# Performance work log

Measured on AMD Instinct MI355X. Metric: run time of the kernel, lower is better.

Reference implementation:

```python
import jax, jax.numpy as jnp
import numpy as np

N_ATOMS = 100000
N_PAIRS = 3200000
N_PROP = 16
N_BASIS = 10
W = 16  # MLP width for pp/pi/ii nodes


def setup_inputs() -> dict:
    key = jax.random.key(0)
    ks = jax.random.split(key, 16)
    s = 0.1
    inp = {
        "ind_2": jax.random.randint(ks[0], (N_PAIRS, 2), 0, N_ATOMS),
        "p1": jax.random.normal(ks[1], (N_ATOMS, N_PROP), dtype=jnp.float32),
        "basis": jax.random.normal(ks[2], (N_PAIRS, N_BASIS), dtype=jnp.float32),
        # pp_pre: [16,16], bias=True
        "Wpre0": jax.random.normal(ks[3], (N_PROP, W), dtype=jnp.float32) * s,
        "bpre0": jnp.zeros((W,), dtype=jnp.float32),
        "Wpre1": jax.random.normal(ks[4], (W, W), dtype=jnp.float32) * s,
        "bpre1": jnp.zeros((W,), dtype=jnp.float32),
        # pi: input 2*W -> W -> W*n_basis, bias=True
        "Wpi0": jax.random.normal(ks[5], (2 * W, W), dtype=jnp.float32) * s,
        "bpi0": jnp.zeros((W,), dtype=jnp.float32),
        "Wpi1": jax.random.normal(ks[6], (W, W * N_BASIS), dtype=jnp.float32) * s,
        "bpi1": jnp.zeros((W * N_BASIS,), dtype=jnp.float32),
        # ii: [16,16], bias=False
        "Wii0": jax.random.normal(ks[7], (W, W), dtype=jnp.float32) * s,
        "Wii1": jax.random.normal(ks[8], (W, W), dtype=jnp.float32) * s,
        # pp_post: [16,16], bias=False
        "Wpost0": jax.random.normal(ks[9], (W, W), dtype=jnp.float32) * s,
        "Wpost1": jax.random.normal(ks[10], (W, W), dtype=jnp.float32) * s,
    }
    return inp


def reference(ind_2, p1, basis, Wpre0, bpre0, Wpre1, bpre1,
              Wpi0, bpi0, Wpi1, bpi1, Wii0, Wii1, Wpost0, Wpost1):
    act = jnp.tanh
    n_atoms = p1.shape[0]
    # pp_pre: per-atom FF (activation on every dense, bias=True)
    p1_in = act(p1 @ Wpre0 + bpre0)
    p1_in = act(p1_in @ Wpre1 + bpre1)
    # PI: gather pair endpoints, concat, MLP, contract with radial basis
    h = jnp.concatenate([p1_in[ind_2[:, 0]], p1_in[ind_2[:, 1]]], axis=-1)  # (P, 2W)
    h = act(h @ Wpi0 + bpi0)                                                # (P, W)
    h = act(h @ Wpi1 + bpi1)                                                # (P, W*n_basis)
    h = h.reshape(h.shape[0], -1, basis.shape[-1])                          # (P, W, n_basis)
    i_pair = jnp.einsum('pcb,pb->pc', h, basis)                             # (P, W)
    # II: pair-mixing FF (bias=False)
    i_pair = act(i_pair @ Wii0)
    i_pair = act(i_pair @ Wii1)
    # IP: scatter-sum pair features back to atoms at ind_2[:,0]
    p_sum = jax.ops.segment_sum(i_pair, ind_2[:, 0], num_segments=n_atoms)  # (A, W)
    # pp_post (bias=False)
    p1_new = act(p_sum @ Wpost0)
    p1_new = act(p1_new @ Wpost1)
    return (p1_new, i_pair)
```

## Files before the change

### kernel.cpp

```cpp
#include <hip/hip_runtime.h>

#define N_ATOMS 100000
#define N_PAIRS 3200000
#define N_PROP 16
#define N_BASIS 10
#define W 16
#define NSUP (N_PAIRS / 32)
#define SCAN_BLK 1024
#define NB ((N_ATOMS + SCAN_BLK - 1) / SCAN_BLK)
#define SC 2.88539008177792681f

typedef short  s16x8  __attribute__((ext_vector_type(8)));
typedef float  f32x4  __attribute__((ext_vector_type(4)));
typedef float  f32x16 __attribute__((ext_vector_type(16)));

__device__ __forceinline__ float tanh_pre(float y) {
    float e = __builtin_amdgcn_exp2f(y);
    return 1.0f - 2.0f * __builtin_amdgcn_rcpf(e + 1.0f);
}
__device__ __forceinline__ float fast_tanh(float x) {
    float e = __builtin_amdgcn_exp2f(x * SC);
    return 1.0f - 2.0f * __builtin_amdgcn_rcpf(e + 1.0f);
}
__device__ __forceinline__ unsigned short bf16r(float f) {
    union { float f; unsigned u; } v; v.f = f;
    unsigned r = v.u + 0x7FFFu + ((v.u >> 16) & 1u);
    return (unsigned short)(r >> 16);
}
__device__ __forceinline__ unsigned cvt_pk_bf16(float a, float b) {
    unsigned r;
    asm("v_cvt_pk_bf16_f32 %0, %1, %2" : "=v"(r) : "v"(a), "v"(b));
    return r;
}
__device__ __forceinline__ float bitf(unsigned u) {
    union { unsigned u; float f; } v; v.u = u; return v.f;
}

__global__ __launch_bounds__(256) void k_pp_pre(
    const float* __restrict__ p1,
    const float* __restrict__ W0, const float* __restrict__ b0,
    const float* __restrict__ W1, const float* __restrict__ b1,
    const float* __restrict__ Wpi0, const float* __restrict__ bpi0,
    float* __restrict__ ytop, float* __restrict__ ybot)
{
    int a = blockIdx.x * 256 + threadIdx.x;
    if (a >= N_ATOMS) return;
    const float4* src = reinterpret_cast<const float4*>(p1 + (size_t)a * N_PROP);
    float4 v0 = src[0], v1 = src[1], v2 = src[2], v3 = src[3];
    float x[N_PROP] = {v0.x,v0.y,v0.z,v0.w, v1.x,v1.y,v1.z,v1.w,
                       v2.x,v2.y,v2.z,v2.w, v3.x,v3.y,v3.z,v3.w};
    float h[W];
#pragma unroll
    for (int c = 0; c < W; ++c) h[c] = b0[c];
#pragma unroll
    for (int k = 0; k < N_PROP; ++k)
#pragma unroll
        for (int c = 0; c < W; ++c) h[c] += x[k] * W0[k*W + c];
#pragma unroll
    for (int c = 0; c < W; ++c) h[c] = fast_tanh(h[c]);
    float y[W];
#pragma unroll
    for (int c = 0; c < W; ++c) y[c] = b1[c];
#pragma unroll
    for (int k = 0; k < W; ++k)
#pragma unroll
        for (int c = 0; c < W; ++c) y[c] += h[k] * W1[k*W + c];
    float t[W];
#pragma unroll
    for (int c = 0; c < W; ++c) t[c] = fast_tanh(y[c]);

    float yt[W], yb[W];
#pragma unroll
    for (int c = 0; c < W; ++c) { yt[c] = bpi0[c]; yb[c] = 0.0f; }
#pragma unroll
    for (int k = 0; k < W; ++k)
#pragma unroll
        for (int c = 0; c < W; ++c) {
            yt[c] += t[k] * Wpi0[k*W + c];
            yb[c] += t[k] * Wpi0[(W + k)*W + c];
        }
    float4* dt = reinterpret_cast<float4*>(ytop + (size_t)a * W);
    float4* db = reinterpret_cast<float4*>(ybot + (size_t)a * W);
#pragma unroll
    for (int q = 0; q < 4; ++q) {
        dt[q] = make_float4(SC*yt[4*q], SC*yt[4*q+1], SC*yt[4*q+2], SC*yt[4*q+3]);
        db[q] = make_float4(SC*yb[4*q], SC*yb[4*q+1], SC*yb[4*q+2], SC*yb[4*q+3]);
    }
}

__global__ __launch_bounds__(256) void k_pair_mfma(
    const int*   __restrict__ ind2,
    const float* __restrict__ basis,
    const float* __restrict__ ytop,
    const float* __restrict__ ybot,
    const float* __restrict__ Wpi1, const float* __restrict__ bpi1,
    const float* __restrict__ Wii0, const float* __restrict__ Wii1,
    float* __restrict__ i_pair_out)
{
    __shared__ s16x8 aw_lds[5][2][32];
    __shared__ s16x8 ab_lds[5][2][32];

    const int lane = threadIdx.x & 63;
    const int wv   = threadIdx.x >> 6;
    const int col  = lane & 31;
    const int h    = lane >> 5;

    for (int e = threadIdx.x; e < 320; e += 256) {
        int T = e >> 6, hh = (e >> 5) & 1, row = e & 31;
        int colW = (4*(row >> 3) + (row & 3)) * N_BASIS + 2*T + ((row >> 2) & 1);
        s16x8 wfrag, bfrag;
#pragma unroll
        for (int j = 0; j < 8; ++j) {
            int k = 8*hh + j;
            wfrag[j] = (short)bf16r(SC * Wpi1[k*(W*N_BASIS) + colW]);
            bfrag[j] = (short)((k == 0) ? bf16r(SC * bpi1[colW]) : 0);
        }
        aw_lds[T][hh][row] = wfrag;
        ab_lds[T][hh][row] = bfrag;
    }

    s16x8 a3, a4;
#pragma unroll
    for (int j = 0; j < 8; ++j) {
        int k = 8*h + j;
        a3[j] = (short)(col < W ? bf16r(SC * Wii0[k*W + col]) : 0);
        a4[j] = (short)(col < W ? bf16r(SC * Wii1[k*W + col]) : 0);
    }
    s16x8 Bones = {0,0,0,0,0,0,0,0};
    if (h == 0) Bones[0] = (short)0x3F80;

    __syncthreads();

    const int stride = gridDim.x * 4;
    int sup = blockIdx.x * 4 + wv;
    if (sup >= NSUP) return;
    const int2* ind2v = reinterpret_cast<const int2*>(ind2);

    int2 ij = ind2v[(size_t)sup * 32 + col];
    f32x4 yt0 = *reinterpret_cast<const f32x4*>(ytop + (size_t)ij.x * W + 8*h);
    f32x4 yt1 = *reinterpret_cast<const f32x4*>(ytop + (size_t)ij.x * W + 8*h + 4);
    f32x4 yb0 = *reinterpret_cast<const f32x4*>(ybot + (size_t)ij.y * W + 8*h);
    f32x4 yb1 = *reinterpret_cast<const f32x4*>(ybot + (size_t)ij.y * W + 8*h + 4);

    for (; sup < NSUP; sup += stride) {
        const int p0 = sup * 32;
        const int p  = p0 + col;
        const int nsup = (sup + stride < NSUP) ? (sup + stride) : sup;

        int2 nij = ind2v[(size_t)nsup * 32 + col];

        float h0[8];
#pragma unroll
        for (int j = 0; j < 4; ++j) h0[j]     = tanh_pre(yt0[j] + yb0[j]);
#pragma unroll
        for (int j = 0; j < 4; ++j) h0[4 + j] = tanh_pre(yt1[j] + yb1[j]);
        unsigned w0h = cvt_pk_bf16(h0[0], h0[1]);
        unsigned w1h = cvt_pk_bf16(h0[2], h0[3]);
        unsigned w2h = cvt_pk_bf16(h0[4], h0[5]);
        unsigned w3h = cvt_pk_bf16(h0[6], h0[7]);
        unsigned w0l = cvt_pk_bf16(h0[0] - bitf(w0h << 16), h0[1] - bitf(w0h & 0xFFFF0000u));
        unsigned w1l = cvt_pk_bf16(h0[2] - bitf(w1h << 16), h0[3] - bitf(w1h & 0xFFFF0000u));
        unsigned w2l = cvt_pk_bf16(h0[4] - bitf(w2h << 16), h0[5] - bitf(w2h & 0xFFFF0000u));
        unsigned w3l = cvt_pk_bf16(h0[6] - bitf(w3h << 16), h0[7] - bitf(w3h & 0xFFFF0000u));
        union { unsigned u[4]; s16x8 v; } BH, BL;
        BH.u[0] = w0h; BH.u[1] = w1h; BH.u[2] = w2h; BH.u[3] = w3h;
        BL.u[0] = w0l; BL.u[1] = w1l; BL.u[2] = w2l; BL.u[3] = w3l;
        s16x8 B2h = BH.v, B2l = BL.v;

        const float2* bb = reinterpret_cast<const float2*>(basis + (size_t)p * N_BASIS);
        float bsel[5];
#pragma unroll
        for (int q = 0; q < 5; ++q) {
            float2 t2 = bb[q];
            bsel[q] = h ? t2.y : t2.x;
        }

        float v[16];
#pragma unroll
        for (int i = 0; i < 16; ++i) v[i] = 0.0f;
#pragma unroll
        for (int T = 0; T < 5; ++T) {
            s16x8 af = aw_lds[T][h][col];
            s16x8 ab = ab_lds[T][h][col];
            f32x16 z = {0.0f};
            z = __builtin_amdgcn_mfma_f32_32x32x16_bf16(ab, Bones, z, 0, 0, 0);
            z = __builtin_amdgcn_mfma_f32_32x32x16_bf16(af, B2h,  z, 0, 0, 0);
            z = __builtin_amdgcn_mfma_f32_32x32x16_bf16(af, B2l,  z, 0, 0, 0);
#pragma unroll
            for (int i = 0; i < 16; ++i)
                v[i] += tanh_pre(z[i]) * bsel[T];
        }

        f32x4 nyt0 = *reinterpret_cast<const f32x4*>(ytop + (size_t)nij.x * W + 8*h);
        f32x4 nyt1 = *reinterpret_cast<const f32x4*>(ytop + (size_t)nij.x * W + 8*h + 4);
        f32x4 nyb0 = *reinterpret_cast<const f32x4*>(ybot + (size_t)nij.y * W + 8*h);
        f32x4 nyb1 = *reinterpret_cast<const f32x4*>(ybot + (size_t)nij.y * W + 8*h + 4);

        float own[8], snd[8];
        if (h == 0) {
#pragma unroll
            for (int j = 0; j < 8; ++j) { own[j] = v[j]; snd[j] = v[8 + j]; }
        } else {
#pragma unroll
            for (int j = 0; j < 8; ++j) { own[j] = v[8 + j]; snd[j] = v[j]; }
        }
        float vf[8];
#pragma unroll
        for (int j = 0; j < 8; ++j) vf[j] = own[j] + __shfl_xor(snd[j], 32);

        union { unsigned u[4]; s16x8 v; } B3u;
        B3u.u[0] = cvt_pk_bf16(vf[0], vf[1]);
        B3u.u[1] = cvt_pk_bf16(vf[2], vf[3]);
        B3u.u[2] = cvt_pk_bf16(vf[4], vf[5]);
        B3u.u[3] = cvt_pk_bf16(vf[6], vf[7]);
        f32x16 ua = {0.0f};
        ua = __builtin_amdgcn_mfma_f32_32x32x16_bf16(a3, B3u.v, ua, 0, 0, 0);
        float u[8];
#pragma unroll
        for (int i = 0; i < 8; ++i) u[i] = tanh_pre(ua[i]);

        float uo[4], us[4];
        if (h == 0) {
#pragma unroll
            for (int j = 0; j < 4; ++j) { uo[j] = u[j]; us[j] = u[4 + j]; }
        } else {
#pragma unroll
            for (int j = 0; j < 4; ++j) { uo[j] = u[4 + j]; us[j] = u[j]; }
        }
        float ur[4];
#pragma unroll
        for (int j = 0; j < 4; ++j) ur[j] = __shfl_xor(us[j], 32);
        union { unsigned u[4]; s16x8 v; } B4u;
        if (h == 0) {
            B4u.u[0] = cvt_pk_bf16(uo[0], uo[1]);
            B4u.u[1] = cvt_pk_bf16(uo[2], uo[3]);
            B4u.u[2] = cvt_pk_bf16(ur[0], ur[1]);
            B4u.u[3] = cvt_pk_bf16(ur[2], ur[3]);
        } else {
            B4u.u[0] = cvt_pk_bf16(ur[0], ur[1]);
            B4u.u[1] = cvt_pk_bf16(ur[2], ur[3]);
            B4u.u[2] = cvt_pk_bf16(uo[0], uo[1]);
            B4u.u[3] = cvt_pk_bf16(uo[2], uo[3]);
        }
        f32x16 wa = {0.0f};
        wa = __builtin_amdgcn_mfma_f32_32x32x16_bf16(a4, B4u.v, wa, 0, 0, 0);
        float wq[8];
#pragma unroll
        for (int i = 0; i < 8; ++i) wq[i] = tanh_pre(wa[i]);

        const int rk0 = lane & 15;
        const int q   = lane >> 4;
#pragma unroll
        for (int k = 0; k < 2; ++k) {
            int row = 16*k + rk0;
            int src = row + 32*(q & 1);
            float vA0 = __shfl(wq[0], src), vA1 = __shfl(wq[1], src);
            float vA2 = __shfl(wq[2], src), vA3 = __shfl(wq[3], src);
            float vB0 = __shfl(wq[4], src), vB1 = __shfl(wq[5], src);
            float vB2 = __shfl(wq[6], src), vB3 = __shfl(wq[7], src);
            bool hiq = (q >= 2);
            f32x4 val = { hiq ? vB0 : vA0, hiq ? vB1 : vA1,
                          hiq ? vB2 : vA2, hiq ? vB3 : vA3 };
            *reinterpret_cast<f32x4*>(i_pair_out + (size_t)(p0 + row) * W + q*4) = val;
        }

        ij = nij;
        yt0 = nyt0; yt1 = nyt1; yb0 = nyb0; yb1 = nyb1;
    }
}

__global__ __launch_bounds__(256) void k_count(const int* __restrict__ ind2,
                                               unsigned* __restrict__ counts,
                                               unsigned* __restrict__ rank)
{
    int t = blockIdx.x * 256 + threadIdx.x;
    if (t >= N_PAIRS / 2) return;
    int4 ii = reinterpret_cast<const int4*>(ind2)[t];
    unsigned r0 = atomicAdd(&counts[ii.x], 1u);
    unsigned r1 = atomicAdd(&counts[ii.z], 1u);
    uint2 rr; rr.x = r0; rr.y = r1;
    *reinterpret_cast<uint2*>(rank + 2*t) = rr;
}

__global__ __launch_bounds__(SCAN_BLK) void k_scanA(const unsigned* __restrict__ counts,
                                                    unsigned* __restrict__ starts,
                                                    unsigned* __restrict__ bsum)
{
    __shared__ unsigned sc[SCAN_BLK];
    int a = blockIdx.x * SCAN_BLK + threadIdx.x;
    unsigned c = (a < N_ATOMS) ? counts[a] : 0u;
    sc[threadIdx.x] = c;
    __syncthreads();
    for (int off = 1; off < SCAN_BLK; off <<= 1) {
        unsigned v = sc[threadIdx.x];
        unsigned add = (threadIdx.x >= off) ? sc[threadIdx.x - off] : 0u;
        __syncthreads();
        sc[threadIdx.x] = v + add;
        __syncthreads();
    }
    if (a < N_ATOMS) starts[a] = sc[threadIdx.x] - c;
    if (threadIdx.x == SCAN_BLK - 1) bsum[blockIdx.x] = sc[SCAN_BLK - 1];
}

__global__ __launch_bounds__(SCAN_BLK) void k_scanC(unsigned* __restrict__ starts,
                                                    const unsigned* __restrict__ bsum)
{
    __shared__ unsigned s[128];
    if (threadIdx.x < 128)
        s[threadIdx.x] = (threadIdx.x < NB) ? bsum[threadIdx.x] : 0u;
    __syncthreads();
    for (int off = 1; off < 128; off <<= 1) {
        unsigned x = (threadIdx.x < 128) ? s[threadIdx.x] : 0u;
        unsigned add = (threadIdx.x >= off && threadIdx.x < 128) ? s[threadIdx.x - off] : 0u;
        __syncthreads();
        if (threadIdx.x < 128) s[threadIdx.x] = x + add;
        __syncthreads();
    }
    unsigned boffb = (blockIdx.x == 0) ? 0u : s[blockIdx.x - 1];
    int a = blockIdx.x * SCAN_BLK + threadIdx.x;
    if (a < N_ATOMS) starts[a] += boffb;
}

__global__ __launch_bounds__(256) void k_sidx(const int* __restrict__ ind2,
                                              const unsigned* __restrict__ rank,
                                              const unsigned* __restrict__ starts,
                                              unsigned* __restrict__ sidx)
{
    int t = blockIdx.x * 256 + threadIdx.x;
    if (t >= N_PAIRS / 2) return;
    int4 ii = reinterpret_cast<const int4*>(ind2)[t];
    uint2 rr = *reinterpret_cast<const uint2*>(rank + 2*t);
    sidx[starts[ii.x] + rr.x] = (unsigned)(2*t);
    sidx[starts[ii.z] + rr.y] = (unsigned)(2*t + 1);
}

__global__ __launch_bounds__(256) void k_reduce_gather(const unsigned* __restrict__ starts,
                                                       const unsigned* __restrict__ counts,
                                                       const unsigned* __restrict__ sidx,
                                                       const float* __restrict__ i_pair,
                                                       float* __restrict__ p_sum)
{
    int a = blockIdx.x * 4 + (threadIdx.x >> 6);
    if (a >= N_ATOMS) return;
    int lane = threadIdx.x & 63;
    int c4 = lane & 3;
    int q  = lane >> 2;
    unsigned n = counts[a], st = starts[a];
    f32x4 acc = {0.f, 0.f, 0.f, 0.f};
    for (unsigned k = q; k < n; k += 16) {
        unsigned pid = sidx[st + k];
        acc += *reinterpret_cast<const f32x4*>(i_pair + (size_t)pid * W + c4*4);
    }
#pragma unroll
    for (int off = 4; off < 64; off <<= 1) {
        acc[0] += __shfl_xor(acc[0], off);
        acc[1] += __shfl_xor(acc[1], off);
        acc[2] += __shfl_xor(acc[2], off);
        acc[3] += __shfl_xor(acc[3], off);
    }
    if (lane < 4)
        *reinterpret_cast<f32x4*>(p_sum + (size_t)a * W + lane*4) = acc;
}

__global__ __launch_bounds__(256) void k_pp_post(
    const float* __restrict__ p_sum,
    const float* __restrict__ W0, const float* __restrict__ W1,
    float* __restrict__ p1_new)
{
    int a = blockIdx.x * 256 + threadIdx.x;
    if (a >= N_ATOMS) return;
    const float4* src = reinterpret_cast<const float4*>(p_sum + (size_t)a * W);
    float4 v0 = src[0], v1 = src[1], v2 = src[2], v3 = src[3];
    float x[W] = {v0.x,v0.y,v0.z,v0.w, v1.x,v1.y,v1.z,v1.w,
                  v2.x,v2.y,v2.z,v2.w, v3.x,v3.y,v3.z,v3.w};
    float h[W];
#pragma unroll
    for (int c = 0; c < W; ++c) h[c] = 0.0f;
#pragma unroll
    for (int k = 0; k < W; ++k)
#pragma unroll
        for (int c = 0; c < W; ++c) h[c] += x[k] * W0[k*W + c];
#pragma unroll
    for (int c = 0; c < W; ++c) h[c] = fast_tanh(h[c]);
    float y[W];
#pragma unroll
    for (int c = 0; c < W; ++c) y[c] = 0.0f;
#pragma unroll
    for (int k = 0; k < W; ++k)
#pragma unroll
        for (int c = 0; c < W; ++c) y[c] += h[k] * W1[k*W + c];
    float4* dst = reinterpret_cast<float4*>(p1_new + (size_t)a * W);
    dst[0] = make_float4(fast_tanh(y[0]),  fast_tanh(y[1]),  fast_tanh(y[2]),  fast_tanh(y[3]));
    dst[1] = make_float4(fast_tanh(y[4]),  fast_tanh(y[5]),  fast_tanh(y[6]),  fast_tanh(y[7]));
    dst[2] = make_float4(fast_tanh(y[8]),  fast_tanh(y[9]),  fast_tanh(y[10]), fast_tanh(y[11]));
    dst[3] = make_float4(fast_tanh(y[12]), fast_tanh(y[13]), fast_tanh(y[14]), fast_tanh(y[15]));
}

extern "C" void kernel_launch(void* const* d_in, const int* in_sizes, int n_in,
                              void* d_out, int out_size, void* d_ws, size_t ws_size,
                              hipStream_t stream) {
    const int*   ind2   = (const int*)d_in[0];
    const float* p1     = (const float*)d_in[1];
    const float* basis  = (const float*)d_in[2];
    const float* Wpre0  = (const float*)d_in[3];
    const float* bpre0  = (const float*)d_in[4];
    const float* Wpre1  = (const float*)d_in[5];
    const float* bpre1  = (const float*)d_in[6];
    const float* Wpi0   = (const float*)d_in[7];
    const float* bpi0   = (const float*)d_in[8];
    const float* Wpi1   = (const float*)d_in[9];
    const float* bpi1   = (const float*)d_in[10];
    const float* Wii0   = (const float*)d_in[11];
    const float* Wii1   = (const float*)d_in[12];
    const float* Wpost0 = (const float*)d_in[13];
    const float* Wpost1 = (const float*)d_in[14];

    float* out    = (float*)d_out;
    float* p1_new = out;
    float* i_pair = out + (size_t)N_ATOMS * W;

    char* ws = (char*)d_ws;
    float*    ytop   = (float*)ws;                                ws += (size_t)N_ATOMS * W * 4;
    float*    ybot   = (float*)ws;                                ws += (size_t)N_ATOMS * W * 4;
    float*    p_sum  = (float*)ws;                                ws += (size_t)N_ATOMS * W * 4;
    unsigned* counts = (unsigned*)ws;                             ws += (size_t)N_ATOMS * 4;
    unsigned* starts = (unsigned*)ws;                             ws += (size_t)N_ATOMS * 4;
    unsigned* bsum   = (unsigned*)ws;                             ws += 1024 * 4;
    unsigned* rank   = (unsigned*)ws;                             ws += (size_t)N_PAIRS * 4;
    unsigned* sidx   = (unsigned*)ws;                             ws += (size_t)N_PAIRS * 4;

    hipMemsetAsync(counts, 0, (size_t)N_ATOMS * sizeof(unsigned), stream);
    k_pp_pre<<<(N_ATOMS + 255) / 256, 256, 0, stream>>>(p1, Wpre0, bpre0, Wpre1, bpre1,
                                                        Wpi0, bpi0, ytop, ybot);
    k_count<<<(N_PAIRS / 2 + 255) / 256, 256, 0, stream>>>(ind2, counts, rank);
    k_scanA<<<NB, SCAN_BLK, 0, stream>>>(counts, starts, bsum);
    k_scanC<<<NB, SCAN_BLK, 0, stream>>>(starts, bsum);
    k_sidx<<<(N_PAIRS / 2 + 255) / 256, 256, 0, stream>>>(ind2, rank, starts, sidx);

    k_pair_mfma<<<2560, 256, 0, stream>>>(ind2, basis, ytop, ybot,
                                          Wpi1, bpi1, Wii0, Wii1, i_pair);
    k_reduce_gather<<<(N_ATOMS + 3) / 4, 256, 0, stream>>>(starts, counts, sidx, i_pair, p_sum);
    k_pp_post<<<(N_ATOMS + 255) / 256, 256, 0, stream>>>(p_sum, Wpost0, Wpost1, p1_new);
}
```

Baseline: 481.9 us.

## Scatter pair features into atom-sorted padded buffer, drop sidx indirection

When the workspace is large enough, the pair kernel also writes each pair's feature row directly into its sorted position (starts + rank) in a padded 32-float-wide buffer. The reduction kernel can then read contiguous rows without going through the sidx index array, and the separate k_sidx kernel is skipped. The cost is an extra 3.2M x 128-byte scattered write, half of it zero padding, which adds substantial write traffic. If the workspace is too small, the old path runs instead.

```diff
diff --git a/kernel.cpp b/kernel.cpp
--- a/kernel.cpp
+++ b/kernel.cpp
@@ -5,6 +5,7 @@
 #define N_PROP 16
 #define N_BASIS 10
 #define W 16
+#define PADW 32
 #define NSUP (N_PAIRS / 32)
 #define SCAN_BLK 1024
 #define NB ((N_ATOMS + SCAN_BLK - 1) / SCAN_BLK)
@@ -88,6 +89,7 @@
     }
 }
 
+template<int PAD>
 __global__ __launch_bounds__(256) void k_pair_mfma(
     const int*   __restrict__ ind2,
     const float* __restrict__ basis,
@@ -95,7 +97,10 @@
     const float* __restrict__ ybot,
     const float* __restrict__ Wpi1, const float* __restrict__ bpi1,
     const float* __restrict__ Wii0, const float* __restrict__ Wii1,
-    float* __restrict__ i_pair_out)
+    float* __restrict__ i_pair_out,
+    const unsigned* __restrict__ starts,
+    const unsigned* __restrict__ rank,
+    float* __restrict__ svals)
 {
     __shared__ s16x8 aw_lds[5][2][32];
     __shared__ s16x8 ab_lds[5][2][32];
@@ -264,6 +269,29 @@
             *reinterpret_cast<f32x4*>(i_pair_out + (size_t)(p0 + row) * W + q*4) = val;
         }
 
+        if (PAD) {
+            unsigned pos = starts[ij.x] + rank[p];
+#pragma unroll
+            for (int k = 0; k < 4; ++k) {
+                int row = 8*k + (lane >> 3);
+                int c   = lane & 7;
+                int src = row + 32*(c & 1);
+                float s0 = __shfl(wq[0], src), s1 = __shfl(wq[1], src);
+                float s2 = __shfl(wq[2], src), s3 = __shfl(wq[3], src);
+                float s4 = __shfl(wq[4], src), s5 = __shfl(wq[5], src);
+                float s6 = __shfl(wq[6], src), s7 = __shfl(wq[7], src);
+                bool hi = (c & 2) != 0;
+                f32x4 val;
+                if (c < 4)
+                    val = (f32x4){ hi ? s4 : s0, hi ? s5 : s1,
+                                   hi ? s6 : s2, hi ? s7 : s3 };
+                else
+                    val = (f32x4){0.f, 0.f, 0.f, 0.f};
+                unsigned posr = (unsigned)__shfl((int)pos, row);
+                *reinterpret_cast<f32x4*>(svals + (size_t)posr * PADW + c*4) = val;
+            }
+        }
+
         ij = nij;
         yt0 = nyt0; yt1 = nyt1; yb0 = nyb0; yb1 = nyb1;
     }
@@ -332,6 +360,31 @@
     uint2 rr = *reinterpret_cast<const uint2*>(rank + 2*t);
     sidx[starts[ii.x] + rr.x] = (unsigned)(2*t);
     sidx[starts[ii.z] + rr.y] = (unsigned)(2*t + 1);
+}
+
+__global__ __launch_bounds__(256) void k_reduce_pad(const unsigned* __restrict__ starts,
+                                                    const unsigned* __restrict__ counts,
+                                                    const float* __restrict__ svals,
+                                                    float* __restrict__ p_sum)
+{
+    int a = blockIdx.x * 4 + (threadIdx.x >> 6);
+    if (a >= N_ATOMS) return;
+    int lane = threadIdx.x & 63;
+    int c4 = lane & 3;
+    int q  = lane >> 2;
+    unsigned n = counts[a], st = starts[a];
+    f32x4 acc = {0.f, 0.f, 0.f, 0.f};
+    for (unsigned k = q; k < n; k += 16)
+        acc += *reinterpret_cast<const f32x4*>(svals + (size_t)(st + k) * PADW + c4*4);
+#pragma unroll
+    for (int off = 4; off < 64; off <<= 1) {
+        acc[0] += __shfl_xor(acc[0], off);
+        acc[1] += __shfl_xor(acc[1], off);
+        acc[2] += __shfl_xor(acc[2], off);
+        acc[3] += __shfl_xor(acc[3], off);
+    }
+    if (lane < 4)
+        *reinterpret_cast<f32x4*>(p_sum + (size_t)a * W + lane*4) = acc;
 }
 
 __global__ __launch_bounds__(256) void k_reduce_gather(const unsigned* __restrict__ starts,
@@ -427,7 +480,12 @@
     unsigned* starts = (unsigned*)ws;                             ws += (size_t)N_ATOMS * 4;
     unsigned* bsum   = (unsigned*)ws;                             ws += 1024 * 4;
     unsigned* rank   = (unsigned*)ws;                             ws += (size_t)N_PAIRS * 4;
-    unsigned* sidx   = (unsigned*)ws;                             ws += (size_t)N_PAIRS * 4;
+    char*     tailp  = ws;
+    float*    svals  = (float*)tailp;
+    unsigned* sidx   = (unsigned*)tailp;
+
+    size_t base = (size_t)(tailp - (char*)d_ws);
+    int use_pad = (ws_size >= base + (size_t)N_PAIRS * PADW * sizeof(float));
 
     hipMemsetAsync(counts, 0, (size_t)N_ATOMS * sizeof(unsigned), stream);
     k_pp_pre<<<(N_ATOMS + 255) / 256, 256, 0, stream>>>(p1, Wpre0, bpre0, Wpre1, bpre1,
@@ -435,10 +493,18 @@
     k_count<<<(N_PAIRS / 2 + 255) / 256, 256, 0, stream>>>(ind2, counts, rank);
     k_scanA<<<NB, SCAN_BLK, 0, stream>>>(counts, starts, bsum);
     k_scanC<<<NB, SCAN_BLK, 0, stream>>>(starts, bsum);
-    k_sidx<<<(N_PAIRS / 2 + 255) / 256, 256, 0, stream>>>(ind2, rank, starts, sidx);
-
-    k_pair_mfma<<<2560, 256, 0, stream>>>(ind2, basis, ytop, ybot,
-                                          Wpi1, bpi1, Wii0, Wii1, i_pair);
-    k_reduce_gather<<<(N_ATOMS + 3) / 4, 256, 0, stream>>>(starts, counts, sidx, i_pair, p_sum);
+
+    if (use_pad) {
+        k_pair_mfma<1><<<2560, 256, 0, stream>>>(ind2, basis, ytop, ybot,
+                                                 Wpi1, bpi1, Wii0, Wii1,
+                                                 i_pair, starts, rank, svals);
+        k_reduce_pad<<<(N_ATOMS + 3) / 4, 256, 0, stream>>>(starts, counts, svals, p_sum);
+    } else {
+        k_sidx<<<(N_PAIRS / 2 + 255) / 256, 256, 0, stream>>>(ind2, rank, starts, sidx);
+        k_pair_mfma<0><<<2560, 256, 0, stream>>>(ind2, basis, ytop, ybot,
+                                                 Wpi1, bpi1, Wii0, Wii1,
+                                                 i_pair, starts, rank, svals);
+        k_reduce_gather<<<(N_ATOMS + 3) / 4, 256, 0, stream>>>(starts, counts, sidx, i_pair, p_sum);
+    }
     k_pp_post<<<(N_ATOMS + 255) / 256, 256, 0, stream>>>(p_sum, Wpost0, Wpost1, p1_new);
 }
```

Result: slower. 562.8 us (+16.8%).

## Fuse pre/count, sidx/pair, and reduce/post kernels; prefetch sidx in reduce

Applied to the files above, without the earlier changes.

Cuts the launch sequence from eight kernels to five. The pp_pre MLP is merged into the count kernel, the sidx scatter is folded into the front of the pair MFMA kernel, and the pp_post MLP is merged into the gather-reduce. The reduce loop now prefetches sorted pair indices two iterations ahead to hide dependent-load latency, and the p_sum round trip through global memory is gone. In exchange, the fused kernels mix workloads of different shapes (the pre MLP runs only in the first N_ATOMS threads of a larger grid), and the post MLP now runs one wave per atom with many shuffles.

```diff
diff --git a/kernel.cpp b/kernel.cpp
--- a/kernel.cpp
+++ b/kernel.cpp
@@ -36,250 +36,67 @@
     union { unsigned u; float f; } v; v.u = u; return v.f;
 }
 
-__global__ __launch_bounds__(256) void k_pp_pre(
+__global__ __launch_bounds__(256) void k_pre_count(
     const float* __restrict__ p1,
     const float* __restrict__ W0, const float* __restrict__ b0,
     const float* __restrict__ W1, const float* __restrict__ b1,
     const float* __restrict__ Wpi0, const float* __restrict__ bpi0,
-    float* __restrict__ ytop, float* __restrict__ ybot)
-{
-    int a = blockIdx.x * 256 + threadIdx.x;
-    if (a >= N_ATOMS) return;
-    const float4* src = reinterpret_cast<const float4*>(p1 + (size_t)a * N_PROP);
-    float4 v0 = src[0], v1 = src[1], v2 = src[2], v3 = src[3];
-    float x[N_PROP] = {v0.x,v0.y,v0.z,v0.w, v1.x,v1.y,v1.z,v1.w,
-                       v2.x,v2.y,v2.z,v2.w, v3.x,v3.y,v3.z,v3.w};
-    float h[W];
-#pragma unroll
-    for (int c = 0; c < W; ++c) h[c] = b0[c];
-#pragma unroll
-    for (int k = 0; k < N_PROP; ++k)
-#pragma unroll
-        for (int c = 0; c < W; ++c) h[c] += x[k] * W0[k*W + c];
-#pragma unroll
-    for (int c = 0; c < W; ++c) h[c] = fast_tanh(h[c]);
-    float y[W];
-#pragma unroll
-    for (int c = 0; c < W; ++c) y[c] = b1[c];
-#pragma unroll
-    for (int k = 0; k < W; ++k)
-#pragma unroll
-        for (int c = 0; c < W; ++c) y[c] += h[k] * W1[k*W + c];
-    float t[W];
-#pragma unroll
-    for (int c = 0; c < W; ++c) t[c] = fast_tanh(y[c]);
-
-    float yt[W], yb[W];
-#pragma unroll
-    for (int c = 0; c < W; ++c) { yt[c] = bpi0[c]; yb[c] = 0.0f; }
-#pragma unroll
-    for (int k = 0; k < W; ++k)
-#pragma unroll
-        for (int c = 0; c < W; ++c) {
-            yt[c] += t[k] * Wpi0[k*W + c];
-            yb[c] += t[k] * Wpi0[(W + k)*W + c];
-        }
-    float4* dt = reinterpret_cast<float4*>(ytop + (size_t)a * W);
-    float4* db = reinterpret_cast<float4*>(ybot + (size_t)a * W);
-#pragma unroll
-    for (int q = 0; q < 4; ++q) {
-        dt[q] = make_float4(SC*yt[4*q], SC*yt[4*q+1], SC*yt[4*q+2], SC*yt[4*q+3]);
-        db[q] = make_float4(SC*yb[4*q], SC*yb[4*q+1], SC*yb[4*q+2], SC*yb[4*q+3]);
-    }
-}
-
-__global__ __launch_bounds__(256) void k_pair_mfma(
-    const int*   __restrict__ ind2,
-    const float* __restrict__ basis,
-    const float* __restrict__ ytop,
-    const float* __restrict__ ybot,
-    const float* __restrict__ Wpi1, const float* __restrict__ bpi1,
-    const float* __restrict__ Wii0, const float* __restrict__ Wii1,
-    float* __restrict__ i_pair_out)
-{
-    __shared__ s16x8 aw_lds[5][2][32];
-    __shared__ s16x8 ab_lds[5][2][32];
-
-    const int lane = threadIdx.x & 63;
-    const int wv   = threadIdx.x >> 6;
-    const int col  = lane & 31;
-    const int h    = lane >> 5;
-
-    for (int e = threadIdx.x; e < 320; e += 256) {
-        int T = e >> 6, hh = (e >> 5) & 1, row = e & 31;
-        int colW = (4*(row >> 3) + (row & 3)) * N_BASIS + 2*T + ((row >> 2) & 1);
-        s16x8 wfrag, bfrag;
-#pragma unroll
-        for (int j = 0; j < 8; ++j) {
-            int k = 8*hh + j;
-            wfrag[j] = (short)bf16r(SC * Wpi1[k*(W*N_BASIS) + colW]);
-            bfrag[j] = (short)((k == 0) ? bf16r(SC * bpi1[colW]) : 0);
-        }
-        aw_lds[T][hh][row] = wfrag;
-        ab_lds[T][hh][row] = bfrag;
-    }
-
-    s16x8 a3, a4;
-#pragma unroll
-    for (int j = 0; j < 8; ++j) {
-        int k = 8*h + j;
-        a3[j] = (short)(col < W ? bf16r(SC * Wii0[k*W + col]) : 0);
-        a4[j] = (short)(col < W ? bf16r(SC * Wii1[k*W + col]) : 0);
-    }
-    s16x8 Bones = {0,0,0,0,0,0,0,0};
-    if (h == 0) Bones[0] = (short)0x3F80;
-
-    __syncthreads();
-
-    const int stride = gridDim.x * 4;
-    int sup = blockIdx.x * 4 + wv;
-    if (sup >= NSUP) return;
-    const int2* ind2v = reinterpret_cast<const int2*>(ind2);
-
-    int2 ij = ind2v[(size_t)sup * 32 + col];
-    f32x4 yt0 = *reinterpret_cast<const f32x4*>(ytop + (size_t)ij.x * W + 8*h);
-    f32x4 yt1 = *reinterpret_cast<const f32x4*>(ytop + (size_t)ij.x * W + 8*h + 4);
-    f32x4 yb0 = *reinterpret_cast<const f32x4*>(ybot + (size_t)ij.y * W + 8*h);
-    f32x4 yb1 = *reinterpret_cast<const f32x4*>(ybot + (size_t)ij.y * W + 8*h + 4);
-
-    for (; sup < NSUP; sup += stride) {
-        const int p0 = sup * 32;
-        const int p  = p0 + col;
-        const int nsup = (sup + stride < NSUP) ? (sup + stride) : sup;
-
-        int2 nij = ind2v[(size_t)nsup * 32 + col];
-
-        float h0[8];
-#pragma unroll
-        for (int j = 0; j < 4; ++j) h0[j]     = tanh_pre(yt0[j] + yb0[j]);
-#pragma unroll
-        for (int j = 0; j < 4; ++j) h0[4 + j] = tanh_pre(yt1[j] + yb1[j]);
-        unsigned w0h = cvt_pk_bf16(h0[0], h0[1]);
-        unsigned w1h = cvt_pk_bf16(h0[2], h0[3]);
-        unsigned w2h = cvt_pk_bf16(h0[4], h0[5]);
-        unsigned w3h = cvt_pk_bf16(h0[6], h0[7]);
-        unsigned w0l = cvt_pk_bf16(h0[0] - bitf(w0h << 16), h0[1] - bitf(w0h & 0xFFFF0000u));
-        unsigned w1l = cvt_pk_bf16(h0[2] - bitf(w1h << 16), h0[3] - bitf(w1h & 0xFFFF0000u));
-        unsigned w2l = cvt_pk_bf16(h0[4] - bitf(w2h << 16), h0[5] - bitf(w2h & 0xFFFF0000u));
-        unsigned w3l = cvt_pk_bf16(h0[6] - bitf(w3h << 16), h0[7] - bitf(w3h & 0xFFFF0000u));
-        union { unsigned u[4]; s16x8 v; } BH, BL;
-        BH.u[0] = w0h; BH.u[1] = w1h; BH.u[2] = w2h; BH.u[3] = w3h;
-        BL.u[0] = w0l; BL.u[1] = w1l; BL.u[2] = w2l; BL.u[3] = w3l;
-        s16x8 B2h = BH.v, B2l = BL.v;
-
-        const float2* bb = reinterpret_cast<const float2*>(basis + (size_t)p * N_BASIS);
-        float bsel[5];
-#pragma unroll
-        for (int q = 0; q < 5; ++q) {
-            float2 t2 = bb[q];
-            bsel[q] = h ? t2.y : t2.x;
-        }
-
-        float v[16];
-#pragma unroll
-        for (int i = 0; i < 16; ++i) v[i] = 0.0f;
-#pragma unroll
-        for (int T = 0; T < 5; ++T) {
-            s16x8 af = aw_lds[T][h][col];
-            s16x8 ab = ab_lds[T][h][col];
-            f32x16 z = {0.0f};
-            z = __builtin_amdgcn_mfma_f32_32x32x16_bf16(ab, Bones, z, 0, 0, 0);
-            z = __builtin_amdgcn_mfma_f32_32x32x16_bf16(af, B2h,  z, 0, 0, 0);
-            z = __builtin_amdgcn_mfma_f32_32x32x16_bf16(af, B2l,  z, 0, 0, 0);
-#pragma unroll
-            for (int i = 0; i < 16; ++i)
-                v[i] += tanh_pre(z[i]) * bsel[T];
-        }
-
-        f32x4 nyt0 = *reinterpret_cast<const f32x4*>(ytop + (size_t)nij.x * W + 8*h);
-        f32x4 nyt1 = *reinterpret_cast<const f32x4*>(ytop + (size_t)nij.x * W + 8*h + 4);
-        f32x4 nyb0 = *reinterpret_cast<const f32x4*>(ybot + (size_t)nij.y * W + 8*h);
-        f32x4 nyb1 = *reinterpret_cast<const f32x4*>(ybot + (size_t)nij.y * W + 8*h + 4);
-
-        float own[8], snd[8];
-        if (h == 0) {
-#pragma unroll
-            for (int j = 0; j < 8; ++j) { own[j] = v[j]; snd[j] = v[8 + j]; }
-        } else {
-#pragma unroll
-            for (int j = 0; j < 8; ++j) { own[j] = v[8 + j]; snd[j] = v[j]; }
-        }
-        float vf[8];
-#pragma unroll
-        for (int j = 0; j < 8; ++j) vf[j] = own[j] + __shfl_xor(snd[j], 32);
-
-        union { unsigned u[4]; s16x8 v; } B3u;
-        B3u.u[0] = cvt_pk_bf16(vf[0], vf[1]);
-        B3u.u[1] = cvt_pk_bf16(vf[2], vf[3]);
-        B3u.u[2] = cvt_pk_bf16(vf[4], vf[5]);
-        B3u.u[3] = cvt_pk_bf16(vf[6], vf[7]);
-        f32x16 ua = {0.0f};
-        ua = __builtin_amdgcn_mfma_f32_32x32x16_bf16(a3, B3u.v, ua, 0, 0, 0);
-        float u[8];
-#pragma unroll
-        for (int i = 0; i < 8; ++i) u[i] = tanh_pre(ua[i]);
-
-        float uo[4], us[4];
-        if (h == 0) {
-#pragma unroll
-            for (int j = 0; j < 4; ++j) { uo[j] = u[j]; us[j] = u[4 + j]; }
-        } else {
-#pragma unroll
-            for (int j = 0; j < 4; ++j) { uo[j] = u[4 + j]; us[j] = u[j]; }
-        }
-        float ur[4];
-#pragma unroll
-        for (int j = 0; j < 4; ++j) ur[j] = __shfl_xor(us[j], 32);
-        union { unsigned u[4]; s16x8 v; } B4u;
-        if (h == 0) {
-            B4u.u[0] = cvt_pk_bf16(uo[0], uo[1]);
-            B4u.u[1] = cvt_pk_bf16(uo[2], uo[3]);
-            B4u.u[2] = cvt_pk_bf16(ur[0], ur[1]);
-            B4u.u[3] = cvt_pk_bf16(ur[2], ur[3]);
-        } else {
-            B4u.u[0] = cvt_pk_bf16(ur[0], ur[1]);
-            B4u.u[1] = cvt_pk_bf16(ur[2], ur[3]);
-            B4u.u[2] = cvt_pk_bf16(uo[0], uo[1]);
-            B4u.u[3] = cvt_pk_bf16(uo[2], uo[3]);
-        }
-        f32x16 wa = {0.0f};
-        wa = __builtin_amdgcn_mfma_f32_32x32x16_bf16(a4, B4u.v, wa, 0, 0, 0);
-        float wq[8];
-#pragma unroll
-        for (int i = 0; i < 8; ++i) wq[i] = tanh_pre(wa[i]);
-
-        const int rk0 = lane & 15;
-        const int q   = lane >> 4;
-#pragma unroll
-        for (int k = 0; k < 2; ++k) {
-            int row = 16*k + rk0;
-            int src = row + 32*(q & 1);
-            float vA0 = __shfl(wq[0], src), vA1 = __shfl(wq[1], src);
-            float vA2 = __shfl(wq[2], src), vA3 = __shfl(wq[3], src);
-            float vB0 = __shfl(wq[4], src), vB1 = __shfl(wq[5], src);
-            float vB2 = __shfl(wq[6], src), vB3 = __shfl(wq[7], src);
-            bool hiq = (q >= 2);
-            f32x4 val = { hiq ? vB0 : vA0, hiq ? vB1 : vA1,
-                          hiq ? vB2 : vA2, hiq ? vB3 : vA3 };
-            *reinterpret_cast<f32x4*>(i_pair_out + (size_t)(p0 + row) * W + q*4) = val;
-        }
-
-        ij = nij;
-        yt0 = nyt0; yt1 = nyt1; yb0 = nyb0; yb1 = nyb1;
-    }
-}
-
-__global__ __launch_bounds__(256) void k_count(const int* __restrict__ ind2,
-                                               unsigned* __restrict__ counts,
-                                               unsigned* __restrict__ rank)
+    float* __restrict__ ytop, float* __restrict__ ybot,
+    const int* __restrict__ ind2,
+    unsigned* __restrict__ counts, unsigned* __restrict__ rank)
 {
     int t = blockIdx.x * 256 + threadIdx.x;
-    if (t >= N_PAIRS / 2) return;
-    int4 ii = reinterpret_cast<const int4*>(ind2)[t];
-    unsigned r0 = atomicAdd(&counts[ii.x], 1u);
-    unsigned r1 = atomicAdd(&counts[ii.z], 1u);
-    uint2 rr; rr.x = r0; rr.y = r1;
-    *reinterpret_cast<uint2*>(rank + 2*t) = rr;
+    if (t < N_PAIRS / 2) {
+        int4 ii = reinterpret_cast<const int4*>(ind2)[t];
+        unsigned r0 = atomicAdd(&counts[ii.x], 1u);
+        unsigned r1 = atomicAdd(&counts[ii.z], 1u);
+        uint2 rr; rr.x = r0; rr.y = r1;
+        *reinterpret_cast<uint2*>(rank + 2*t) = rr;
+    }
+    if (t < N_ATOMS) {
+        int a = t;
+        const float4* src = reinterpret_cast<const float4*>(p1 + (size_t)a * N_PROP);
+        float4 v0 = src[0], v1 = src[1], v2 = src[2], v3 = src[3];
+        float x[N_PROP] = {v0.x,v0.y,v0.z,v0.w, v1.x,v1.y,v1.z,v1.w,
+                           v2.x,v2.y,v2.z,v2.w, v3.x,v3.y,v3.z,v3.w};
+        float h[W];
+#pragma unroll
+        for (int c = 0; c < W; ++c) h[c] = b0[c];
+#pragma unroll
+        for (int k = 0; k < N_PROP; ++k)
+#pragma unroll
+            for (int c = 0; c < W; ++c) h[c] += x[k] * W0[k*W + c];
+#pragma unroll
+        for (int c = 0; c < W; ++c) h[c] = fast_tanh(h[c]);
+        float y[W];
+#pragma unroll
+        for (int c = 0; c < W; ++c) y[c] = b1[c];
+#pragma unroll
+        for (int k = 0; k < W; ++k)
+#pragma unroll
+            for (int c = 0; c < W; ++c) y[c] += h[k] * W1[k*W + c];
+        float tt[W];
+#pragma unroll
+        for (int c = 0; c < W; ++c) tt[c] = fast_tanh(y[c]);
+
+        float yt[W], yb[W];
+#pragma unroll
+        for (int c = 0; c < W; ++c) { yt[c] = bpi0[c]; yb[c] = 0.0f; }
+#pragma unroll
+        for (int k = 0; k < W; ++k)
+#pragma unroll
+            for (int c = 0; c < W; ++c) {
+                yt[c] += tt[k] * Wpi0[k*W + c];
+                yb[c] += tt[k] * Wpi0[(W + k)*W + c];
+            }
+        float4* dt = reinterpret_cast<float4*>(ytop + (size_t)a * W);
+        float4* db = reinterpret_cast<float4*>(ybot + (size_t)a * W);
+#pragma unroll
+        for (int q = 0; q < 4; ++q) {
+            dt[q] = make_float4(SC*yt[4*q], SC*yt[4*q+1], SC*yt[4*q+2], SC*yt[4*q+3]);
+            db[q] = make_float4(SC*yb[4*q], SC*yb[4*q+1], SC*yb[4*q+2], SC*yb[4*q+3]);
+        }
+    }
 }
 
 __global__ __launch_bounds__(SCAN_BLK) void k_scanA(const unsigned* __restrict__ counts,
@@ -321,24 +138,204 @@
     if (a < N_ATOMS) starts[a] += boffb;
 }
 
-__global__ __launch_bounds__(256) void k_sidx(const int* __restrict__ ind2,
-                                              const unsigned* __restrict__ rank,
-                                              const unsigned* __restrict__ starts,
-                                              unsigned* __restrict__ sidx)
+__global__ __launch_bounds__(256) void k_pair_mfma(
+    const int*   __restrict__ ind2,
+    const float* __restrict__ basis,
+    const float* __restrict__ ytop,
+    const float* __restrict__ ybot,
+    const float* __restrict__ Wpi1, const float* __restrict__ bpi1,
+    const float* __restrict__ Wii0, const float* __restrict__ Wii1,
+    float* __restrict__ i_pair_out,
+    const unsigned* __restrict__ starts,
+    const unsigned* __restrict__ rank,
+    unsigned* __restrict__ sidx)
 {
-    int t = blockIdx.x * 256 + threadIdx.x;
-    if (t >= N_PAIRS / 2) return;
-    int4 ii = reinterpret_cast<const int4*>(ind2)[t];
-    uint2 rr = *reinterpret_cast<const uint2*>(rank + 2*t);
-    sidx[starts[ii.x] + rr.x] = (unsigned)(2*t);
-    sidx[starts[ii.z] + rr.y] = (unsigned)(2*t + 1);
-}
-
-__global__ __launch_bounds__(256) void k_reduce_gather(const unsigned* __restrict__ starts,
-                                                       const unsigned* __restrict__ counts,
-                                                       const unsigned* __restrict__ sidx,
-                                                       const float* __restrict__ i_pair,
-                                                       float* __restrict__ p_sum)
+    __shared__ s16x8 aw_lds[5][2][32];
+    __shared__ s16x8 ab_lds[5][2][32];
+
+    for (int t = blockIdx.x * 256 + threadIdx.x; t < N_PAIRS / 2; t += gridDim.x * 256) {
+        int4 ii = reinterpret_cast<const int4*>(ind2)[t];
+        uint2 rr = *reinterpret_cast<const uint2*>(rank + 2*t);
+        sidx[starts[ii.x] + rr.x] = (unsigned)(2*t);
+        sidx[starts[ii.z] + rr.y] = (unsigned)(2*t + 1);
+    }
+
+    const int lane = threadIdx.x & 63;
+    const int wv   = threadIdx.x >> 6;
+    const int col  = lane & 31;
+    const int h    = lane >> 5;
+
+    for (int e = threadIdx.x; e < 320; e += 256) {
+        int T = e >> 6, hh = (e >> 5) & 1, row = e & 31;
+        int colW = (4*(row >> 3) + (row & 3)) * N_BASIS + 2*T + ((row >> 2) & 1);
+        s16x8 wfrag, bfrag;
+#pragma unroll
+        for (int j = 0; j < 8; ++j) {
+            int k = 8*hh + j;
+            wfrag[j] = (short)bf16r(SC * Wpi1[k*(W*N_BASIS) + colW]);
+            bfrag[j] = (short)((k == 0) ? bf16r(SC * bpi1[colW]) : 0);
+        }
+        aw_lds[T][hh][row] = wfrag;
+        ab_lds[T][hh][row] = bfrag;
+    }
+
+    s16x8 a3, a4;
+#pragma unroll
+    for (int j = 0; j < 8; ++j) {
+        int k = 8*h + j;
+        a3[j] = (short)(col < W ? bf16r(SC * Wii0[k*W + col]) : 0);
+        a4[j] = (short)(col < W ? bf16r(SC * Wii1[k*W + col]) : 0);
+    }
+    s16x8 Bones = {0,0,0,0,0,0,0,0};
+    if (h == 0) Bones[0] = (short)0x3F80;
+
+    __syncthreads();
+
+    const int stride = gridDim.x * 4;
+    int sup = blockIdx.x * 4 + wv;
+    if (sup >= NSUP) return;
+    const int2* ind2v = reinterpret_cast<const int2*>(ind2);
+
+    int2 ij = ind2v[(size_t)sup * 32 + col];
+    f32x4 yt0 = *reinterpret_cast<const f32x4*>(ytop + (size_t)ij.x * W + 8*h);
+    f32x4 yt1 = *reinterpret_cast<const f32x4*>(ytop + (size_t)ij.x * W + 8*h + 4);
+    f32x4 yb0 = *reinterpret_cast<const f32x4*>(ybot + (size_t)ij.y * W + 8*h);
+    f32x4 yb1 = *reinterpret_cast<const f32x4*>(ybot + (size_t)ij.y * W + 8*h + 4);
+
+    for (; sup < NSUP; sup += stride) {
+        const int p0 = sup * 32;
+        const int p  = p0 + col;
+        const int nsup = (sup + stride < NSUP) ? (sup + stride) : sup;
+
+        int2 nij = ind2v[(size_t)nsup * 32 + col];
+
+        float h0[8];
+#pragma unroll
+        for (int j = 0; j < 4; ++j) h0[j]     = tanh_pre(yt0[j] + yb0[j]);
+#pragma unroll
+        for (int j = 0; j < 4; ++j) h0[4 + j] = tanh_pre(yt1[j] + yb1[j]);
+        unsigned w0h = cvt_pk_bf16(h0[0], h0[1]);
+        unsigned w1h = cvt_pk_bf16(h0[2], h0[3]);
+        unsigned w2h = cvt_pk_bf16(h0[4], h0[5]);
+        unsigned w3h = cvt_pk_bf16(h0[6], h0[7]);
+        unsigned w0l = cvt_pk_bf16(h0[0] - bitf(w0h << 16), h0[1] - bitf(w0h & 0xFFFF0000u));
+        unsigned w1l = cvt_pk_bf16(h0[2] - bitf(w1h << 16), h0[3] - bitf(w1h & 0xFFFF0000u));
+        unsigned w2l = cvt_pk_bf16(h0[4] - bitf(w2h << 16), h0[5] - bitf(w2h & 0xFFFF0000u));
+        unsigned w3l = cvt_pk_bf16(h0[6] - bitf(w3h << 16), h0[7] - bitf(w3h & 0xFFFF0000u));
+        union { unsigned u[4]; s16x8 v; } BH, BL;
+        BH.u[0] = w0h; BH.u[1] = w1h; BH.u[2] = w2h; BH.u[3] = w3h;
+        BL.u[0] = w0l; BL.u[1] = w1l; BL.u[2] = w2l; BL.u[3] = w3l;
+        s16x8 B2h = BH.v, B2l = BL.v;
+
+        const float2* bb = reinterpret_cast<const float2*>(basis + (size_t)p * N_BASIS);
+        float bsel[5];
+#pragma unroll
+        for (int q = 0; q < 5; ++q) {
+            float2 t2 = bb[q];
+            bsel[q] = h ? t2.y : t2.x;
+        }
+
+        float v[16];
+#pragma unroll
+        for (int i = 0; i < 16; ++i) v[i] = 0.0f;
+#pragma unroll
+        for (int T = 0; T < 5; ++T) {
+            s16x8 af = aw_lds[T][h][col];
+            s16x8 ab = ab_lds[T][h][col];
+            f32x16 z = {0.0f};
+            z = __builtin_amdgcn_mfma_f32_32x32x16_bf16(ab, Bones, z, 0, 0, 0);
+            z = __builtin_amdgcn_mfma_f32_32x32x16_bf16(af, B2h,  z, 0, 0, 0);
+            z = __builtin_amdgcn_mfma_f32_32x32x16_bf16(af, B2l,  z, 0, 0, 0);
+#pragma unroll
+            for (int i = 0; i < 16; ++i)
+                v[i] += tanh_pre(z[i]) * bsel[T];
+        }
+
+        f32x4 nyt0 = *reinterpret_cast<const f32x4*>(ytop + (size_t)nij.x * W + 8*h);
+        f32x4 nyt1 = *reinterpret_cast<const f32x4*>(ytop + (size_t)nij.x * W + 8*h + 4);
+        f32x4 nyb0 = *reinterpret_cast<const f32x4*>(ybot + (size_t)nij.y * W + 8*h);
+        f32x4 nyb1 = *reinterpret_cast<const f32x4*>(ybot + (size_t)nij.y * W + 8*h + 4);
+
+        float own[8], snd[8];
+        if (h == 0) {
+#pragma unroll
+            for (int j = 0; j < 8; ++j) { own[j] = v[j]; snd[j] = v[8 + j]; }
+        } else {
+#pragma unroll
+            for (int j = 0; j < 8; ++j) { own[j] = v[8 + j]; snd[j] = v[j]; }
+        }
+        float vf[8];
+#pragma unroll
+        for (int j = 0; j < 8; ++j) vf[j] = own[j] + __shfl_xor(snd[j], 32);
+
+        union { unsigned u[4]; s16x8 v; } B3u;
+        B3u.u[0] = cvt_pk_bf16(vf[0], vf[1]);
+        B3u.u[1] = cvt_pk_bf16(vf[2], vf[3]);
+        B3u.u[2] = cvt_pk_bf16(vf[4], vf[5]);
+        B3u.u[3] = cvt_pk_bf16(vf[6], vf[7]);
+        f32x16 ua = {0.0f};
+        ua = __builtin_amdgcn_mfma_f32_32x32x16_bf16(a3, B3u.v, ua, 0, 0, 0);
+        float u[8];
+#pragma unroll
+        for (int i = 0; i < 8; ++i) u[i] = tanh_pre(ua[i]);
+
+        float uo[4], us[4];
+        if (h == 0) {
+#pragma unroll
+            for (int j = 0; j < 4; ++j) { uo[j] = u[j]; us[j] = u[4 + j]; }
+        } else {
+#pragma unroll
+            for (int j = 0; j < 4; ++j) { uo[j] = u[4 + j]; us[j] = u[j]; }
+        }
+        float ur[4];
+#pragma unroll
+        for (int j = 0; j < 4; ++j) ur[j] = __shfl_xor(us[j], 32);
+        union { unsigned u[4]; s16x8 v; } B4u;
+        if (h == 0) {
+            B4u.u[0] = cvt_pk_bf16(uo[0], uo[1]);
+            B4u.u[1] = cvt_pk_bf16(uo[2], uo[3]);
+            B4u.u[2] = cvt_pk_bf16(ur[0], ur[1]);
+            B4u.u[3] = cvt_pk_bf16(ur[2], ur[3]);
+        } else {
+            B4u.u[0] = cvt_pk_bf16(ur[0], ur[1]);
+            B4u.u[1] = cvt_pk_bf16(ur[2], ur[3]);
+            B4u.u[2] = cvt_pk_bf16(uo[0], uo[1]);
+            B4u.u[3] = cvt_pk_bf16(uo[2], uo[3]);
+        }
+        f32x16 wa = {0.0f};
+        wa = __builtin_amdgcn_mfma_f32_32x32x16_bf16(a4, B4u.v, wa, 0, 0, 0);
+        float wq[8];
+#pragma unroll
+        for (int i = 0; i < 8; ++i) wq[i] = tanh_pre(wa[i]);
+
+        const int rk0 = lane & 15;
+        const int q   = lane >> 4;
+#pragma unroll
+        for (int k = 0; k < 2; ++k) {
+            int row = 16*k + rk0;
+            int src = row + 32*(q & 1);
+            float vA0 = __shfl(wq[0], src), vA1 = __shfl(wq[1], src);
+            float vA2 = __shfl(wq[2], src), vA3 = __shfl(wq[3], src);
+            float vB0 = __shfl(wq[4], src), vB1 = __shfl(wq[5], src);
+            float vB2 = __shfl(wq[6], src), vB3 = __shfl(wq[7], src);
+            bool hiq = (q >= 2);
+            f32x4 val = { hiq ? vB0 : vA0, hiq ? vB1 : vA1,
+                          hiq ? vB2 : vA2, hiq ? vB3 : vA3 };
+            *reinterpret_cast<f32x4*>(i_pair_out + (size_t)(p0 + row) * W + q*4) = val;
+        }
+
+        ij = nij;
+        yt0 = nyt0; yt1 = nyt1; yb0 = nyb0; yb1 = nyb1;
+    }
+}
+
+__global__ __launch_bounds__(256) void k_reduce_post(
+    const unsigned* __restrict__ starts,
+    const unsigned* __restrict__ counts,
+    const unsigned* __restrict__ sidx,
+    const float* __restrict__ i_pair,
+    const float* __restrict__ W0, const float* __restrict__ W1,
+    float* __restrict__ p1_new)
 {
     int a = blockIdx.x * 4 + (threadIdx.x >> 6);
     if (a >= N_ATOMS) return;
@@ -347,9 +344,17 @@
     int q  = lane >> 2;
     unsigned n = counts[a], st = starts[a];
     f32x4 acc = {0.f, 0.f, 0.f, 0.f};
-    for (unsigned k = q; k < n; k += 16) {
-        unsigned pid = sidx[st + k];
-        acc += *reinterpret_cast<const f32x4*>(i_pair + (size_t)pid * W + c4*4);
+    if (n > 0) {
+        unsigned nm1 = n - 1;
+        unsigned pidA = sidx[st + ((unsigned)q < n ? (unsigned)q : nm1)];
+        unsigned pidB = sidx[st + ((unsigned)(q + 16) < n ? (unsigned)(q + 16) : nm1)];
+        for (unsigned k = q; k < n; k += 16) {
+            f32x4 r = *reinterpret_cast<const f32x4*>(i_pair + (size_t)pidA * W + c4*4);
+            unsigned kc = k + 32;
+            unsigned pidC = sidx[st + (kc < n ? kc : nm1)];
+            acc += r;
+            pidA = pidB; pidB = pidC;
+        }
     }
 #pragma unroll
     for (int off = 4; off < 64; off <<= 1) {
@@ -358,42 +363,24 @@
         acc[2] += __shfl_xor(acc[2], off);
         acc[3] += __shfl_xor(acc[3], off);
     }
-    if (lane < 4)
-        *reinterpret_cast<f32x4*>(p_sum + (size_t)a * W + lane*4) = acc;
-}
-
-__global__ __launch_bounds__(256) void k_pp_post(
-    const float* __restrict__ p_sum,
-    const float* __restrict__ W0, const float* __restrict__ W1,
-    float* __restrict__ p1_new)
-{
-    int a = blockIdx.x * 256 + threadIdx.x;
-    if (a >= N_ATOMS) return;
-    const float4* src = reinterpret_cast<const float4*>(p_sum + (size_t)a * W);
-    float4 v0 = src[0], v1 = src[1], v2 = src[2], v3 = src[3];
-    float x[W] = {v0.x,v0.y,v0.z,v0.w, v1.x,v1.y,v1.z,v1.w,
-                  v2.x,v2.y,v2.z,v2.w, v3.x,v3.y,v3.z,v3.w};
-    float h[W];
-#pragma unroll
-    for (int c = 0; c < W; ++c) h[c] = 0.0f;
-#pragma unroll
-    for (int k = 0; k < W; ++k)
-#pragma unroll
-        for (int c = 0; c < W; ++c) h[c] += x[k] * W0[k*W + c];
-#pragma unroll
-    for (int c = 0; c < W; ++c) h[c] = fast_tanh(h[c]);
-    float y[W];
-#pragma unroll
-    for (int c = 0; c < W; ++c) y[c] = 0.0f;
-#pragma unroll
-    for (int k = 0; k < W; ++k)
-#pragma unroll
-        for (int c = 0; c < W; ++c) y[c] += h[k] * W1[k*W + c];
-    float4* dst = reinterpret_cast<float4*>(p1_new + (size_t)a * W);
-    dst[0] = make_float4(fast_tanh(y[0]),  fast_tanh(y[1]),  fast_tanh(y[2]),  fast_tanh(y[3]));
-    dst[1] = make_float4(fast_tanh(y[4]),  fast_tanh(y[5]),  fast_tanh(y[6]),  fast_tanh(y[7]));
-    dst[2] = make_float4(fast_tanh(y[8]),  fast_tanh(y[9]),  fast_tanh(y[10]), fast_tanh(y[11]));
-    dst[3] = make_float4(fast_tanh(y[12]), fast_tanh(y[13]), fast_tanh(y[14]), fast_tanh(y[15]));
+    float ps[16];
+#pragma unroll
+    for (int c = 0; c < 16; ++c)
+        ps[c] = __shfl(acc[c & 3], c >> 2);
+
+    int cm = lane & 15;
+    float hv = 0.f;
+#pragma unroll
+    for (int k = 0; k < W; ++k) hv += ps[k] * W0[k*W + cm];
+    hv = fast_tanh(hv);
+    float hh[16];
+#pragma unroll
+    for (int c = 0; c < 16; ++c) hh[c] = __shfl(hv, c);
+    float yv = 0.f;
+#pragma unroll
+    for (int k = 0; k < W; ++k) yv += hh[k] * W1[k*W + cm];
+    yv = fast_tanh(yv);
+    if (lane < 16) p1_new[(size_t)a * W + lane] = yv;
 }
 
 extern "C" void kernel_launch(void* const* d_in, const int* in_sizes, int n_in,
@@ -422,7 +409,6 @@
     char* ws = (char*)d_ws;
     float*    ytop   = (float*)ws;                                ws += (size_t)N_ATOMS * W * 4;
     float*    ybot   = (float*)ws;                                ws += (size_t)N_ATOMS * W * 4;
-    float*    p_sum  = (float*)ws;                                ws += (size_t)N_ATOMS * W * 4;
     unsigned* counts = (unsigned*)ws;                             ws += (size_t)N_ATOMS * 4;
     unsigned* starts = (unsigned*)ws;                             ws += (size_t)N_ATOMS * 4;
     unsigned* bsum   = (unsigned*)ws;                             ws += 1024 * 4;
@@ -430,15 +416,13 @@
     unsigned* sidx   = (unsigned*)ws;                             ws += (size_t)N_PAIRS * 4;
 
     hipMemsetAsync(counts, 0, (size_t)N_ATOMS * sizeof(unsigned), stream);
-    k_pp_pre<<<(N_ATOMS + 255) / 256, 256, 0, stream>>>(p1, Wpre0, bpre0, Wpre1, bpre1,
-                                                        Wpi0, bpi0, ytop, ybot);
-    k_count<<<(N_PAIRS / 2 + 255) / 256, 256, 0, stream>>>(ind2, counts, rank);
+    k_pre_count<<<(N_PAIRS / 2 + 255) / 256, 256, 0, stream>>>(
+        p1, Wpre0, bpre0, Wpre1, bpre1, Wpi0, bpi0, ytop, ybot, ind2, counts, rank);
     k_scanA<<<NB, SCAN_BLK, 0, stream>>>(counts, starts, bsum);
     k_scanC<<<NB, SCAN_BLK, 0, stream>>>(starts, bsum);
-    k_sidx<<<(N_PAIRS / 2 + 255) / 256, 256, 0, stream>>>(ind2, rank, starts, sidx);
-
     k_pair_mfma<<<2560, 256, 0, stream>>>(ind2, basis, ytop, ybot,
-                                          Wpi1, bpi1, Wii0, Wii1, i_pair);
-    k_reduce_gather<<<(N_ATOMS + 3) / 4, 256, 0, stream>>>(starts, counts, sidx, i_pair, p_sum);
-    k_pp_post<<<(N_ATOMS + 255) / 256, 256, 0, stream>>>(p_sum, Wpost0, Wpost1, p1_new);
-}
+                                          Wpi1, bpi1, Wii0, Wii1,
+                                          i_pair, starts, rank, sidx);
+    k_reduce_post<<<(N_ATOMS + 3) / 4, 256, 0, stream>>>(starts, counts, sidx, i_pair,
+                                                         Wpost0, Wpost1, p1_new);
+}
```

Measured after the change: 485.6 us. No clear change (+0.8%).
